# Optimization experiments

Hardware: AMD Instinct MI355X
Metric: run time of the kernel (lower is better)

The kernel has to match this reference:

```python
import jax, jax.numpy as jnp
import numpy as np

UNITS = 256
NUM_HEADS = 8
HEAD_DIM = UNITS // NUM_HEADS
B, N = 8, 2048


def setup_inputs() -> dict:
    key = jax.random.key(0)
    ks = jax.random.split(key, 7)
    node_features = jax.random.normal(ks[0], (B, N, UNITS), dtype=jnp.float32)
    adjacency_matrix = jax.random.randint(ks[1], (B, N, N), 0, 2, dtype=jnp.int32)
    # Glorot-ish scaled dense weights
    s = 1.0 / np.sqrt(UNITS)
    Wq = jax.random.normal(ks[2], (UNITS, UNITS), dtype=jnp.float32) * s
    Wk = jax.random.normal(ks[3], (UNITS, UNITS), dtype=jnp.float32) * s
    Wv = jax.random.normal(ks[4], (UNITS, UNITS), dtype=jnp.float32) * s
    Wo = jax.random.normal(ks[5], (UNITS, UNITS), dtype=jnp.float32) * s
    bo = jnp.zeros((UNITS,), dtype=jnp.float32)
    return {"node_features": node_features, "adjacency_matrix": adjacency_matrix,
            "Wq": Wq, "Wk": Wk, "Wv": Wv, "Wo": Wo, "bo": bo}


def reference(node_features, adjacency_matrix, Wq, Wk, Wv, Wo, bo):
    b, n, _ = node_features.shape
    h, d = NUM_HEADS, HEAD_DIM
    # projections -> [b, h, n, d]
    q = (node_features @ Wq).reshape(b, n, h, d).transpose(0, 2, 1, 3)
    k = (node_features @ Wk).reshape(b, n, h, d).transpose(0, 2, 1, 3)
    v = (node_features @ Wv).reshape(b, n, h, d).transpose(0, 2, 1, 3)
    scores = jnp.einsum('bhqd,bhkd->bhqk', q, k) / jnp.sqrt(jnp.float32(d))
    mask = adjacency_matrix[:, None, :, :] > 0  # [b,1,n,n] broadcasts over heads
    scores = jnp.where(mask, scores, jnp.float32(-1e9))
    w = jax.nn.softmax(scores, axis=-1)
    # dropout is identity at inference (training=None)
    ctx = jnp.einsum('bhqk,bhkd->bhqd', w, v)
    ctx = ctx.transpose(0, 2, 1, 3).reshape(b, n, h * d)
    return ctx @ Wo + bo
```

## Files before the change

kernel.cpp:

```cpp
#include <hip/hip_runtime.h>
#include <cstdint>
#include <cstddef>

#define B_ 8
#define N_ 2048
#define H_ 8
#define D_ 32
#define U_ 256

typedef _Float16 half8 __attribute__((ext_vector_type(8)));
typedef _Float16 half4 __attribute__((ext_vector_type(4)));
typedef float float4v __attribute__((ext_vector_type(4)));

__device__ __forceinline__ float fast_exp2(float x) {
#if __has_builtin(__builtin_amdgcn_exp2f)
  return __builtin_amdgcn_exp2f(x);
#else
  return exp2f(x);
#endif
}

__global__ __launch_bounds__(256)
void k_prep(const float* __restrict__ X,
            const float* __restrict__ Wq, const float* __restrict__ Wk,
            const float* __restrict__ Wv, const float* __restrict__ Wo,
            _Float16* __restrict__ Xh, _Float16* __restrict__ WT)
{
  const int bid = blockIdx.x, tid = threadIdx.x;
  if (bid < 512) {
    const size_t base = ((size_t)bid * 256 + tid) * 32;
    const float* src = X + base;
    _Float16* dst = Xh + base;
#pragma unroll
    for (int i = 0; i < 4; ++i) {
      float4v a = *(const float4v*)(src + i * 8);
      float4v b = *(const float4v*)(src + i * 8 + 4);
      half8 h;
      h[0] = (_Float16)a[0]; h[1] = (_Float16)a[1];
      h[2] = (_Float16)a[2]; h[3] = (_Float16)a[3];
      h[4] = (_Float16)b[0]; h[5] = (_Float16)b[1];
      h[6] = (_Float16)b[2]; h[7] = (_Float16)b[3];
      *(half8*)(dst + i * 8) = h;
    }
  } else {
    const int m = bid - 512;
    const float* W = (m == 0) ? Wq : (m == 1) ? Wk : (m == 2) ? Wv : Wo;
    const float scale = (m == 0) ? 0.25505413f : 1.0f;
    _Float16* T = WT + (size_t)m * U_ * U_;
    __shared__ _Float16 Ts[64][72];
    const int r = tid >> 2, seg = tid & 3;
    for (int t = 0; t < 16; ++t) {
      const int k0 = (t >> 2) * 64, n0 = (t & 3) * 64;
      float4v a[4];
      const float* s = W + (size_t)(k0 + r) * U_ + n0 + seg * 16;
#pragma unroll
      for (int i = 0; i < 4; ++i) a[i] = *(const float4v*)(s + i * 4);
      __syncthreads();
#pragma unroll
      for (int i = 0; i < 4; ++i)
#pragma unroll
        for (int j = 0; j < 4; ++j)
          Ts[seg * 16 + i * 4 + j][r] = (_Float16)(a[i][j] * scale);
      __syncthreads();
      _Float16* d = T + (size_t)(n0 + r) * U_ + k0 + seg * 16;
      *(half8*)d       = *(const half8*)&Ts[r][seg * 16];
      *(half8*)(d + 8) = *(const half8*)&Ts[r][seg * 16 + 8];
    }
  }
}

__global__ __launch_bounds__(256, 2)
void k_qkv(const _Float16* __restrict__ Xh, const _Float16* __restrict__ WT,
           _Float16* __restrict__ Qg, _Float16* __restrict__ Kg,
           _Float16* __restrict__ VTg)
{
  __shared__ __attribute__((aligned(16))) _Float16 tr[128 * 136];

  const int tid  = threadIdx.x;
  const int lane = tid & 63;
  const int w    = tid >> 6;
  const int c    = lane & 15;
  const int qd   = lane >> 4;
  const int bx   = blockIdx.x;
  const int proj = bx >> 1;
  const int n0l  = (bx & 1) * 128;
  const int m0   = blockIdx.y * 128;

  const _Float16* Wp = WT + (size_t)proj * U_ * U_;
  const _Float16* arow0 = Xh + (size_t)(m0 + w * 32 + c) * U_ + qd * 8;
  const _Float16* arow1 = arow0 + (size_t)16 * U_;
  const _Float16* brow  = Wp + (size_t)(n0l + c) * U_ + qd * 8;

  const float4v zero4 = {0.f, 0.f, 0.f, 0.f};
  float4v acc[2][8];
#pragma unroll
  for (int i = 0; i < 2; ++i)
#pragma unroll
    for (int j = 0; j < 8; ++j) acc[i][j] = zero4;

#pragma unroll 2
  for (int ks = 0; ks < 8; ++ks) {
    const int k0 = ks * 32;
    half8 af0 = *(const half8*)(arow0 + k0);
    half8 af1 = *(const half8*)(arow1 + k0);
    half8 bf[8];
#pragma unroll
    for (int nt = 0; nt < 8; ++nt)
      bf[nt] = *(const half8*)(brow + (size_t)nt * 16 * U_ + k0);
#pragma unroll
    for (int nt = 0; nt < 8; ++nt) {
      acc[0][nt] = __builtin_amdgcn_mfma_f32_16x16x32_f16(af0, bf[nt], acc[0][nt], 0, 0, 0);
      acc[1][nt] = __builtin_amdgcn_mfma_f32_16x16x32_f16(af1, bf[nt], acc[1][nt], 0, 0, 0);
    }
  }

  const int b   = m0 >> 11;
  const int nb0 = m0 & (N_ - 1);
  if (proj < 2) {
    _Float16* Og = (proj == 0) ? Qg : Kg;
#pragma unroll
    for (int mt = 0; mt < 2; ++mt)
#pragma unroll
      for (int nt = 0; nt < 8; ++nt)
#pragma unroll
        for (int r = 0; r < 4; ++r) {
          const int rowl = w * 32 + mt * 16 + qd * 4 + r;
          Og[(size_t)(b * N_ + nb0 + rowl) * U_ + n0l + nt * 16 + c] = (_Float16)acc[mt][nt][r];
        }
  } else {
#pragma unroll
    for (int mt = 0; mt < 2; ++mt)
#pragma unroll
      for (int nt = 0; nt < 8; ++nt)
#pragma unroll
        for (int r = 0; r < 4; ++r)
          tr[(nt * 16 + c) * 136 + w * 32 + mt * 16 + qd * 4 + r] = (_Float16)acc[mt][nt][r];
    __syncthreads();
    const int u = tid >> 1;
    const int seg = tid & 1;
    _Float16* dst = VTg + (size_t)(b * U_ + n0l + u) * N_ + nb0 + seg * 64;
#pragma unroll
    for (int i = 0; i < 8; ++i)
      *(half8*)(dst + i * 8) = *(const half8*)&tr[u * 136 + seg * 64 + i * 8];
  }
}

#define KS_H (32 * 264)
#define VT_H (256 * 40)

struct StageRegs {
  half8 k0, k1, v0, v1;
  int a0, a1;
};

__global__ __launch_bounds__(512, 2)
void k_attn(const _Float16* __restrict__ Qg, const _Float16* __restrict__ Kg,
            const _Float16* __restrict__ VTg, const int* __restrict__ Adj,
            _Float16* __restrict__ Cg)
{
  __shared__ __attribute__((aligned(16))) _Float16 KsB[2][KS_H];
  __shared__ __attribute__((aligned(16))) _Float16 VTsB[2][VT_H];
  __shared__ __attribute__((aligned(8)))  unsigned int maskB[2][32];

  const int tid  = threadIdx.x;
  const int lane = tid & 63;
  const int w    = tid >> 6;
  const int c    = lane & 15;
  const int qd   = lane >> 4;
  const int wg   = blockIdx.x;
  const int b    = wg & 7;
  const int q0   = (wg >> 3) * 32;

  const _Float16* kptr = Kg + (size_t)(b * N_ + (tid >> 4)) * U_ + (tid & 15) * 16;
  const _Float16* vptr = VTg + (size_t)(b * U_ + (tid >> 1)) * N_ + (tid & 1) * 16;
  const int rr = lane >> 5;
  const int kk = lane & 31;
  const int* aptr = Adj + (size_t)(b * N_ + q0 + w * 4 + rr) * N_ + kk;

  half8 qb[2];
#pragma unroll
  for (int nt = 0; nt < 2; ++nt)
    qb[nt] = *(const half8*)(Qg + (size_t)(b * N_ + q0 + nt * 16 + c) * U_ + w * D_ + qd * 8);

  const float4v init4 = {-8.f, -8.f, -8.f, -8.f};
  const float4v zero4 = {0.f, 0.f, 0.f, 0.f};
  float4v acc[2][2];
#pragma unroll
  for (int i = 0; i < 2; ++i)
#pragma unroll
    for (int j = 0; j < 2; ++j) acc[i][j] = zero4;
  float lrow[2] = {0.f, 0.f};

  auto load_tile = [&](int kt) -> StageRegs {
    StageRegs r;
    const _Float16* ks = kptr + (size_t)kt * 32 * U_;
    const _Float16* vs = vptr + (size_t)kt * 32;
    const int* as = aptr + (size_t)kt * 32;
    r.k0 = *(const half8*)ks;  r.k1 = *(const half8*)(ks + 8);
    r.v0 = *(const half8*)vs;  r.v1 = *(const half8*)(vs + 8);
    r.a0 = as[0];
    r.a1 = as[2 * N_];
    return r;
  };
  auto store_tile = [&](const StageRegs& r, int buf) {
    _Float16* kd = &KsB[buf][(tid >> 4) * 264 + (tid & 15) * 16];
    *(half8*)kd = r.k0;  *(half8*)(kd + 8) = r.k1;
    _Float16* vd = &VTsB[buf][(tid >> 1) * 40 + (tid & 1) * 16];
    *(half8*)vd = r.v0;  *(half8*)(vd + 8) = r.v1;
    unsigned long long bm;
    bm = __ballot(r.a0 > 0); if (lane == 0) *(unsigned long long*)&maskB[buf][w * 4 + 0] = bm;
    bm = __ballot(r.a1 > 0); if (lane == 0) *(unsigned long long*)&maskB[buf][w * 4 + 2] = bm;
  };
  auto compute_tile = [&](int buf) {
    half8 ka0 = *(const half8*)&KsB[buf][(0 * 16 + c) * 264 + w * D_ + qd * 8];
    half8 ka1 = *(const half8*)&KsB[buf][(1 * 16 + c) * 264 + w * D_ + qd * 8];
    half4 va[2][2];
#pragma unroll
    for (int mt = 0; mt < 2; ++mt)
#pragma unroll
      for (int kc = 0; kc < 2; ++kc)
        va[mt][kc] = *(const half4*)&VTsB[buf][(w * D_ + mt * 16 + c) * 40 + kc * 16 + qd * 4];
#pragma unroll
    for (int nt = 0; nt < 2; ++nt) {
      float4v s0 = __builtin_amdgcn_mfma_f32_16x16x32_f16(ka0, qb[nt], init4, 0, 0, 0);
      float4v s1 = __builtin_amdgcn_mfma_f32_16x16x32_f16(ka1, qb[nt], init4, 0, 0, 0);
      const unsigned int mq = maskB[buf][nt * 16 + c];
      const unsigned int t0 = mq >> (qd * 4);
      const unsigned int t1 = mq >> (16 + qd * 4);
      half4 pb0, pb1;
      float ls = 0.f;
#pragma unroll
      for (int r = 0; r < 4; ++r) {
        float e0 = fast_exp2(s0[r]);
        float e1 = fast_exp2(s1[r]);
        float p0 = ((t0 >> r) & 1u) ? e0 : 0.f;
        float p1 = ((t1 >> r) & 1u) ? e1 : 0.f;
        ls += p0 + p1;
        pb0[r] = (_Float16)p0;
        pb1[r] = (_Float16)p1;
      }
      lrow[nt] += ls;
      acc[0][nt] = __builtin_amdgcn_mfma_f32_16x16x16f16(va[0][0], pb0, acc[0][nt], 0, 0, 0);
      acc[0][nt] = __builtin_amdgcn_mfma_f32_16x16x16f16(va[0][1], pb1, acc[0][nt], 0, 0, 0);
      acc[1][nt] = __builtin_amdgcn_mfma_f32_16x16x16f16(va[1][0], pb0, acc[1][nt], 0, 0, 0);
      acc[1][nt] = __builtin_amdgcn_mfma_f32_16x16x16f16(va[1][1], pb1, acc[1][nt], 0, 0, 0);
    }
  };

  {
    StageRegs r = load_tile(0);
    store_tile(r, 0);
  }
  __syncthreads();

#pragma unroll 1
  for (int kt = 0; kt < 64; kt += 2) {
    {
      StageRegs r = load_tile(kt + 1);
      compute_tile(0);
      store_tile(r, 1);
    }
    __syncthreads();
    if (kt + 2 < 64) {
      StageRegs r = load_tile(kt + 2);
      compute_tile(1);
      store_tile(r, 0);
    } else {
      compute_tile(1);
    }
    __syncthreads();
  }

  float rinv[2];
#pragma unroll
  for (int nt = 0; nt < 2; ++nt) {
    float l = lrow[nt];
    l += __shfl_xor(l, 16, 64);
    l += __shfl_xor(l, 32, 64);
    rinv[nt] = (l > 0.f) ? 1.f / l : 0.f;
  }
  _Float16* ctxS = (_Float16*)KsB;
#pragma unroll
  for (int mt = 0; mt < 2; ++mt)
#pragma unroll
    for (int nt = 0; nt < 2; ++nt) {
      half4 hv;
#pragma unroll
      for (int r = 0; r < 4; ++r)
        hv[r] = (_Float16)(acc[mt][nt][r] * rinv[nt]);
      *(half4*)&ctxS[(nt * 16 + c) * 264 + w * D_ + mt * 16 + qd * 4] = hv;
    }
  __syncthreads();
  {
    const int row = tid >> 4;
    const int seg = tid & 15;
    _Float16* dst = Cg + (size_t)(b * N_ + q0 + row) * U_ + seg * 16;
    *(half8*)dst       = *(const half8*)&ctxS[row * 264 + seg * 16];
    *(half8*)(dst + 8) = *(const half8*)&ctxS[row * 264 + seg * 16 + 8];
  }
}

__global__ __launch_bounds__(256, 2)
void k_out(const _Float16* __restrict__ Cg, const _Float16* __restrict__ WTo,
           const float* __restrict__ bo, float* __restrict__ Out)
{
  const int tid  = threadIdx.x;
  const int lane = tid & 63;
  const int w    = tid >> 6;
  const int c    = lane & 15;
  const int qd   = lane >> 4;
  const int n0l  = blockIdx.x * 128;
  const int m0   = blockIdx.y * 128;

  const _Float16* arow0 = Cg + (size_t)(m0 + w * 32 + c) * U_ + qd * 8;
  const _Float16* arow1 = arow0 + (size_t)16 * U_;
  const _Float16* brow  = WTo + (size_t)(n0l + c) * U_ + qd * 8;

  const float4v zero4 = {0.f, 0.f, 0.f, 0.f};
  float4v acc[2][8];
#pragma unroll
  for (int i = 0; i < 2; ++i)
#pragma unroll
    for (int j = 0; j < 8; ++j) acc[i][j] = zero4;

#pragma unroll 2
  for (int ks = 0; ks < 8; ++ks) {
    const int k0 = ks * 32;
    half8 af0 = *(const half8*)(arow0 + k0);
    half8 af1 = *(const half8*)(arow1 + k0);
    half8 bf[8];
#pragma unroll
    for (int nt = 0; nt < 8; ++nt)
      bf[nt] = *(const half8*)(brow + (size_t)nt * 16 * U_ + k0);
#pragma unroll
    for (int nt = 0; nt < 8; ++nt) {
      acc[0][nt] = __builtin_amdgcn_mfma_f32_16x16x32_f16(af0, bf[nt], acc[0][nt], 0, 0, 0);
      acc[1][nt] = __builtin_amdgcn_mfma_f32_16x16x32_f16(af1, bf[nt], acc[1][nt], 0, 0, 0);
    }
  }

#pragma unroll
  for (int nt = 0; nt < 8; ++nt) {
    const float bias = bo[n0l + nt * 16 + c];
#pragma unroll
    for (int mt = 0; mt < 2; ++mt)
#pragma unroll
      for (int r = 0; r < 4; ++r) {
        const int rowl = w * 32 + mt * 16 + qd * 4 + r;
        Out[(size_t)(m0 + rowl) * U_ + n0l + nt * 16 + c] = acc[mt][nt][r] + bias;
      }
  }
}

extern "C" void kernel_launch(void* const* d_in, const int* in_sizes, int n_in,
                              void* d_out, int out_size, void* d_ws, size_t ws_size,
                              hipStream_t stream) {
  const float* X   = (const float*)d_in[0];
  const int*   Adj = (const int*)d_in[1];
  const float* Wq  = (const float*)d_in[2];
  const float* Wk  = (const float*)d_in[3];
  const float* Wv  = (const float*)d_in[4];
  const float* Wo  = (const float*)d_in[5];
  const float* bo  = (const float*)d_in[6];
  float* Out = (float*)d_out;

  const size_t elems = (size_t)B_ * N_ * U_;
  _Float16* Qg  = (_Float16*)d_ws;
  _Float16* Kg  = Qg + elems;
  _Float16* VTg = Kg + elems;
  _Float16* Xh  = VTg + elems;
  _Float16* Cg  = Xh;
  _Float16* WT  = Xh + elems;

  k_prep<<<dim3(516), 256, 0, stream>>>(X, Wq, Wk, Wv, Wo, Xh, WT);
  k_qkv<<<dim3(6, 128), 256, 0, stream>>>(Xh, WT, Qg, Kg, VTg);
  k_attn<<<dim3(512), 512, 0, stream>>>(Qg, Kg, VTg, Adj, Cg);
  k_out<<<dim3(2, 128), 256, 0, stream>>>(Cg, WT + 3 * U_ * U_, bo, Out);
}
```

Baseline: 361.5 us.

## Single-buffer attention for higher occupancy and swap MFMA operands for vector stores

The attention kernel drops double buffering of its K/V/mask tiles and adds an extra barrier per tile, shrinking shared memory so launch bounds can request up to 8 blocks per CU. The QKV and output GEMMs swap MFMA operand order so each lane holds contiguous output columns, which allows half4/float4 stores and removes the LDS transpose for V^T. The weight-transpose prep is split across 16 blocks instead of 4. The risk is that losing double buffering and adding a sync per tile exposes global load latency, unless the extra occupancy hides it.

```diff
diff --git a/kernel.cpp b/kernel.cpp
--- a/kernel.cpp
+++ b/kernel.cpp
@@ -43,14 +43,16 @@
       *(half8*)(dst + i * 8) = h;
     }
   } else {
-    const int m = bid - 512;
+    const int id = bid - 512;
+    const int m = id >> 2;
+    const int n0 = (id & 3) * 64;
     const float* W = (m == 0) ? Wq : (m == 1) ? Wk : (m == 2) ? Wv : Wo;
     const float scale = (m == 0) ? 0.25505413f : 1.0f;
     _Float16* T = WT + (size_t)m * U_ * U_;
     __shared__ _Float16 Ts[64][72];
     const int r = tid >> 2, seg = tid & 3;
-    for (int t = 0; t < 16; ++t) {
-      const int k0 = (t >> 2) * 64, n0 = (t & 3) * 64;
+    for (int t = 0; t < 4; ++t) {
+      const int k0 = t * 64;
       float4v a[4];
       const float* s = W + (size_t)(k0 + r) * U_ + n0 + seg * 16;
 #pragma unroll
@@ -69,13 +71,11 @@
   }
 }
 
-__global__ __launch_bounds__(256, 2)
+__global__ __launch_bounds__(256, 4)
 void k_qkv(const _Float16* __restrict__ Xh, const _Float16* __restrict__ WT,
            _Float16* __restrict__ Qg, _Float16* __restrict__ Kg,
            _Float16* __restrict__ VTg)
 {
-  __shared__ __attribute__((aligned(16))) _Float16 tr[128 * 136];
-
   const int tid  = threadIdx.x;
   const int lane = tid & 63;
   const int w    = tid >> 6;
@@ -92,11 +92,11 @@
   const _Float16* brow  = Wp + (size_t)(n0l + c) * U_ + qd * 8;
 
   const float4v zero4 = {0.f, 0.f, 0.f, 0.f};
-  float4v acc[2][8];
-#pragma unroll
-  for (int i = 0; i < 2; ++i)
-#pragma unroll
-    for (int j = 0; j < 8; ++j) acc[i][j] = zero4;
+  float4v acc[8][2];
+#pragma unroll
+  for (int i = 0; i < 8; ++i)
+#pragma unroll
+    for (int j = 0; j < 2; ++j) acc[i][j] = zero4;
 
 #pragma unroll 2
   for (int ks = 0; ks < 8; ++ks) {
@@ -107,10 +107,18 @@
 #pragma unroll
     for (int nt = 0; nt < 8; ++nt)
       bf[nt] = *(const half8*)(brow + (size_t)nt * 16 * U_ + k0);
-#pragma unroll
-    for (int nt = 0; nt < 8; ++nt) {
-      acc[0][nt] = __builtin_amdgcn_mfma_f32_16x16x32_f16(af0, bf[nt], acc[0][nt], 0, 0, 0);
-      acc[1][nt] = __builtin_amdgcn_mfma_f32_16x16x32_f16(af1, bf[nt], acc[1][nt], 0, 0, 0);
+    if (proj < 2) {
+#pragma unroll
+      for (int nt = 0; nt < 8; ++nt) {
+        acc[nt][0] = __builtin_amdgcn_mfma_f32_16x16x32_f16(bf[nt], af0, acc[nt][0], 0, 0, 0);
+        acc[nt][1] = __builtin_amdgcn_mfma_f32_16x16x32_f16(bf[nt], af1, acc[nt][1], 0, 0, 0);
+      }
+    } else {
+#pragma unroll
+      for (int nt = 0; nt < 8; ++nt) {
+        acc[nt][0] = __builtin_amdgcn_mfma_f32_16x16x32_f16(af0, bf[nt], acc[nt][0], 0, 0, 0);
+        acc[nt][1] = __builtin_amdgcn_mfma_f32_16x16x32_f16(af1, bf[nt], acc[nt][1], 0, 0, 0);
+      }
     }
   }
 
@@ -119,48 +127,46 @@
   if (proj < 2) {
     _Float16* Og = (proj == 0) ? Qg : Kg;
 #pragma unroll
-    for (int mt = 0; mt < 2; ++mt)
-#pragma unroll
-      for (int nt = 0; nt < 8; ++nt)
-#pragma unroll
-        for (int r = 0; r < 4; ++r) {
-          const int rowl = w * 32 + mt * 16 + qd * 4 + r;
-          Og[(size_t)(b * N_ + nb0 + rowl) * U_ + n0l + nt * 16 + c] = (_Float16)acc[mt][nt][r];
-        }
+    for (int nt = 0; nt < 8; ++nt)
+#pragma unroll
+      for (int mt = 0; mt < 2; ++mt) {
+        half4 hv;
+#pragma unroll
+        for (int r = 0; r < 4; ++r) hv[r] = (_Float16)acc[nt][mt][r];
+        const int seq = nb0 + w * 32 + mt * 16 + c;
+        *(half4*)(Og + (size_t)(b * N_ + seq) * U_ + n0l + nt * 16 + qd * 4) = hv;
+      }
   } else {
 #pragma unroll
-    for (int mt = 0; mt < 2; ++mt)
-#pragma unroll
-      for (int nt = 0; nt < 8; ++nt)
-#pragma unroll
-        for (int r = 0; r < 4; ++r)
-          tr[(nt * 16 + c) * 136 + w * 32 + mt * 16 + qd * 4 + r] = (_Float16)acc[mt][nt][r];
-    __syncthreads();
-    const int u = tid >> 1;
-    const int seg = tid & 1;
-    _Float16* dst = VTg + (size_t)(b * U_ + n0l + u) * N_ + nb0 + seg * 64;
-#pragma unroll
-    for (int i = 0; i < 8; ++i)
-      *(half8*)(dst + i * 8) = *(const half8*)&tr[u * 136 + seg * 64 + i * 8];
+    for (int nt = 0; nt < 8; ++nt)
+#pragma unroll
+      for (int mt = 0; mt < 2; ++mt) {
+        half4 hv;
+#pragma unroll
+        for (int r = 0; r < 4; ++r) hv[r] = (_Float16)acc[nt][mt][r];
+        const int u = n0l + nt * 16 + c;
+        const int seq = nb0 + w * 32 + mt * 16 + qd * 4;
+        *(half4*)(VTg + (size_t)(b * U_ + u) * N_ + seq) = hv;
+      }
   }
 }
 
 #define KS_H (32 * 264)
-#define VT_H (256 * 40)
+#define VT_H (256 * 36)
 
 struct StageRegs {
   half8 k0, k1, v0, v1;
   int a0, a1;
 };
 
-__global__ __launch_bounds__(512, 2)
+__global__ __launch_bounds__(512, 8)
 void k_attn(const _Float16* __restrict__ Qg, const _Float16* __restrict__ Kg,
             const _Float16* __restrict__ VTg, const int* __restrict__ Adj,
             _Float16* __restrict__ Cg)
 {
-  __shared__ __attribute__((aligned(16))) _Float16 KsB[2][KS_H];
-  __shared__ __attribute__((aligned(16))) _Float16 VTsB[2][VT_H];
-  __shared__ __attribute__((aligned(8)))  unsigned int maskB[2][32];
+  __shared__ __attribute__((aligned(16))) _Float16 Ks[KS_H];
+  __shared__ __attribute__((aligned(16))) _Float16 VTs[VT_H];
+  __shared__ __attribute__((aligned(8)))  unsigned int maskS[32];
 
   const int tid  = threadIdx.x;
   const int lane = tid & 63;
@@ -202,29 +208,29 @@
     r.a1 = as[2 * N_];
     return r;
   };
-  auto store_tile = [&](const StageRegs& r, int buf) {
-    _Float16* kd = &KsB[buf][(tid >> 4) * 264 + (tid & 15) * 16];
+  auto store_tile = [&](const StageRegs& r) {
+    _Float16* kd = &Ks[(tid >> 4) * 264 + (tid & 15) * 16];
     *(half8*)kd = r.k0;  *(half8*)(kd + 8) = r.k1;
-    _Float16* vd = &VTsB[buf][(tid >> 1) * 40 + (tid & 1) * 16];
+    _Float16* vd = &VTs[(tid >> 1) * 36 + (tid & 1) * 16];
     *(half8*)vd = r.v0;  *(half8*)(vd + 8) = r.v1;
     unsigned long long bm;
-    bm = __ballot(r.a0 > 0); if (lane == 0) *(unsigned long long*)&maskB[buf][w * 4 + 0] = bm;
-    bm = __ballot(r.a1 > 0); if (lane == 0) *(unsigned long long*)&maskB[buf][w * 4 + 2] = bm;
+    bm = __ballot(r.a0 > 0); if (lane == 0) *(unsigned long long*)&maskS[w * 4 + 0] = bm;
+    bm = __ballot(r.a1 > 0); if (lane == 0) *(unsigned long long*)&maskS[w * 4 + 2] = bm;
   };
-  auto compute_tile = [&](int buf) {
-    half8 ka0 = *(const half8*)&KsB[buf][(0 * 16 + c) * 264 + w * D_ + qd * 8];
-    half8 ka1 = *(const half8*)&KsB[buf][(1 * 16 + c) * 264 + w * D_ + qd * 8];
+  auto compute_tile = [&]() {
+    half8 ka0 = *(const half8*)&Ks[(0 * 16 + c) * 264 + w * D_ + qd * 8];
+    half8 ka1 = *(const half8*)&Ks[(1 * 16 + c) * 264 + w * D_ + qd * 8];
     half4 va[2][2];
 #pragma unroll
     for (int mt = 0; mt < 2; ++mt)
 #pragma unroll
       for (int kc = 0; kc < 2; ++kc)
-        va[mt][kc] = *(const half4*)&VTsB[buf][(w * D_ + mt * 16 + c) * 40 + kc * 16 + qd * 4];
+        va[mt][kc] = *(const half4*)&VTs[(w * D_ + mt * 16 + c) * 36 + kc * 16 + qd * 4];
 #pragma unroll
     for (int nt = 0; nt < 2; ++nt) {
       float4v s0 = __builtin_amdgcn_mfma_f32_16x16x32_f16(ka0, qb[nt], init4, 0, 0, 0);
       float4v s1 = __builtin_amdgcn_mfma_f32_16x16x32_f16(ka1, qb[nt], init4, 0, 0, 0);
-      const unsigned int mq = maskB[buf][nt * 16 + c];
+      const unsigned int mq = maskS[nt * 16 + c];
       const unsigned int t0 = mq >> (qd * 4);
       const unsigned int t1 = mq >> (16 + qd * 4);
       half4 pb0, pb1;
@@ -249,26 +255,21 @@
 
   {
     StageRegs r = load_tile(0);
-    store_tile(r, 0);
+    store_tile(r);
   }
   __syncthreads();
 
 #pragma unroll 1
-  for (int kt = 0; kt < 64; kt += 2) {
-    {
+  for (int kt = 0; kt < 64; ++kt) {
+    if (kt + 1 < 64) {
       StageRegs r = load_tile(kt + 1);
-      compute_tile(0);
-      store_tile(r, 1);
-    }
-    __syncthreads();
-    if (kt + 2 < 64) {
-      StageRegs r = load_tile(kt + 2);
-      compute_tile(1);
-      store_tile(r, 0);
+      compute_tile();
+      __syncthreads();
+      store_tile(r);
+      __syncthreads();
     } else {
-      compute_tile(1);
-    }
-    __syncthreads();
+      compute_tile();
+    }
   }
 
   float rinv[2];
@@ -279,7 +280,8 @@
     l += __shfl_xor(l, 32, 64);
     rinv[nt] = (l > 0.f) ? 1.f / l : 0.f;
   }
-  _Float16* ctxS = (_Float16*)KsB;
+  __syncthreads();
+  _Float16* ctxS = Ks;
 #pragma unroll
   for (int mt = 0; mt < 2; ++mt)
 #pragma unroll
@@ -300,7 +302,7 @@
   }
 }
 
-__global__ __launch_bounds__(256, 2)
+__global__ __launch_bounds__(256, 4)
 void k_out(const _Float16* __restrict__ Cg, const _Float16* __restrict__ WTo,
            const float* __restrict__ bo, float* __restrict__ Out)
 {
@@ -317,11 +319,11 @@
   const _Float16* brow  = WTo + (size_t)(n0l + c) * U_ + qd * 8;
 
   const float4v zero4 = {0.f, 0.f, 0.f, 0.f};
-  float4v acc[2][8];
-#pragma unroll
-  for (int i = 0; i < 2; ++i)
-#pragma unroll
-    for (int j = 0; j < 8; ++j) acc[i][j] = zero4;
+  float4v acc[8][2];
+#pragma unroll
+  for (int i = 0; i < 8; ++i)
+#pragma unroll
+    for (int j = 0; j < 2; ++j) acc[i][j] = zero4;
 
 #pragma unroll 2
   for (int ks = 0; ks < 8; ++ks) {
@@ -334,21 +336,20 @@
       bf[nt] = *(const half8*)(brow + (size_t)nt * 16 * U_ + k0);
 #pragma unroll
     for (int nt = 0; nt < 8; ++nt) {
-      acc[0][nt] = __builtin_amdgcn_mfma_f32_16x16x32_f16(af0, bf[nt], acc[0][nt], 0, 0, 0);
-      acc[1][nt] = __builtin_amdgcn_mfma_f32_16x16x32_f16(af1, bf[nt], acc[1][nt], 0, 0, 0);
+      acc[nt][0] = __builtin_amdgcn_mfma_f32_16x16x32_f16(bf[nt], af0, acc[nt][0], 0, 0, 0);
+      acc[nt][1] = __builtin_amdgcn_mfma_f32_16x16x32_f16(bf[nt], af1, acc[nt][1], 0, 0, 0);
     }
   }
 
 #pragma unroll
   for (int nt = 0; nt < 8; ++nt) {
-    const float bias = bo[n0l + nt * 16 + c];
-#pragma unroll
-    for (int mt = 0; mt < 2; ++mt)
-#pragma unroll
-      for (int r = 0; r < 4; ++r) {
-        const int rowl = w * 32 + mt * 16 + qd * 4 + r;
-        Out[(size_t)(m0 + rowl) * U_ + n0l + nt * 16 + c] = acc[mt][nt][r] + bias;
-      }
+    const float4v bias = *(const float4v*)(bo + n0l + nt * 16 + qd * 4);
+#pragma unroll
+    for (int mt = 0; mt < 2; ++mt) {
+      const int seq = m0 + w * 32 + mt * 16 + c;
+      float4v v = acc[nt][mt] + bias;
+      *(float4v*)(Out + (size_t)seq * U_ + n0l + nt * 16 + qd * 4) = v;
+    }
   }
 }
 
@@ -372,7 +373,7 @@
   _Float16* Cg  = Xh;
   _Float16* WT  = Xh + elems;
 
-  k_prep<<<dim3(516), 256, 0, stream>>>(X, Wq, Wk, Wv, Wo, Xh, WT);
+  k_prep<<<dim3(528), 256, 0, stream>>>(X, Wq, Wk, Wv, Wo, Xh, WT);
   k_qkv<<<dim3(6, 128), 256, 0, stream>>>(Xh, WT, Qg, Kg, VTg);
   k_attn<<<dim3(512), 512, 0, stream>>>(Qg, Kg, VTg, Adj, Cg);
   k_out<<<dim3(2, 128), 256, 0, stream>>>(Cg, WT + 3 * U_ * U_, bo, Out);
```

Result: slower. 1.042 ms (+188.2%).
